# Kernel optimization log

Hardware: AMD Instinct MI355X
Metric: run time of the kernel (lower is better)

Reference implementation:

```python
import jax, jax.numpy as jnp
import numpy as np

C_IN, H, T_OUT, C_OUT = 16, 256, 24, 8


def setup_inputs() -> dict:
    key = jax.random.key(0)
    ks = jax.random.split(key, 8)
    s_ih = 1.0 / np.sqrt(H)
    x = jax.random.normal(ks[0], (8192, C_IN, 48), dtype=jnp.float32)
    # Encoder LSTMCell params (PyTorch layout: gates stacked [i, f, g, o], each H rows)
    enc_Wih = jax.random.uniform(ks[1], (4 * H, C_IN), minval=-s_ih, maxval=s_ih, dtype=jnp.float32)
    enc_Whh = jax.random.uniform(ks[2], (4 * H, H), minval=-s_ih, maxval=s_ih, dtype=jnp.float32)
    enc_b = jax.random.uniform(ks[3], (4 * H,), minval=-s_ih, maxval=s_ih, dtype=jnp.float32)  # b_ih + b_hh folded
    # Decoder LSTMCell has input_size=0 -> W_ih is (4H, 0), contributes nothing
    dec_Whh = jax.random.uniform(ks[4], (4 * H, H), minval=-s_ih, maxval=s_ih, dtype=jnp.float32)
    dec_b = jax.random.uniform(ks[5], (4 * H,), minval=-s_ih, maxval=s_ih, dtype=jnp.float32)
    # TimestepDense: per-timestep (non-shared) linear H -> C_OUT, dropout inactive at eval
    dense_W = jax.random.uniform(ks[6], (T_OUT, C_OUT, H), minval=-s_ih, maxval=s_ih, dtype=jnp.float32)
    dense_b = jax.random.uniform(ks[7], (T_OUT, C_OUT), minval=-s_ih, maxval=s_ih, dtype=jnp.float32)
    return {"x": x, "enc_Wih": enc_Wih, "enc_Whh": enc_Whh, "enc_b": enc_b,
            "dec_Whh": dec_Whh, "dec_b": dec_b, "dense_W": dense_W, "dense_b": dense_b}


def _lstm_step(h, c, gates):
    i, f, g, o = jnp.split(gates, 4, axis=-1)
    c_new = jax.nn.sigmoid(f) * c + jax.nn.sigmoid(i) * jnp.tanh(g)
    h_new = jax.nn.sigmoid(o) * jnp.tanh(c_new)
    return h_new, c_new


def reference(x, enc_Wih, enc_Whh, enc_b, dec_Whh, dec_b, dense_W, dense_b):
    N = x.shape[0]
    # ----- Encoder: scan over T input steps -----
    xt = jnp.transpose(x, (2, 0, 1))  # (T, N, C)
    h0 = jnp.zeros((N, H), dtype=x.dtype)
    c0 = jnp.zeros((N, H), dtype=x.dtype)

    def enc_step(carry, x_t):
        h, c = carry
        gates = x_t @ enc_Wih.T + h @ enc_Whh.T + enc_b  # (N, 4H)
        h, c = _lstm_step(h, c, gates)
        return (h, c), None

    (h_enc, _), _ = jax.lax.scan(enc_step, (h0, c0), xt)

    # ----- Decoder: zero-input LSTM cell, collect hidden states -----
    def dec_step(carry, _):
        h, c = carry
        gates = h @ dec_Whh.T + dec_b
        h, c = _lstm_step(h, c, gates)
        return (h, c), h

    (_, _), hs = jax.lax.scan(dec_step, (h_enc, c0), None, length=T_OUT)  # hs: (T_OUT, N, H)

    # ----- TimestepDense: per-timestep linear H -> C_OUT (eval mode, dropout off) -----
    out = jnp.einsum('tnh,toh->not', hs, dense_W) + dense_b.T[None]  # (N, C_OUT, T_OUT)
    return out
```

## Files before the change

kernel.cpp:

```cpp
#include <hip/hip_runtime.h>

typedef __attribute__((ext_vector_type(8))) _Float16 f16x8;
typedef __attribute__((ext_vector_type(4))) float    f32x4;

#define HD    256
#define CIN   16
#define TIN   48
#define TOUT  24
#define COUT  8
#define MB    32
#define KPAD  296
#define KT_ENC 9
#define KT_DEC 8
#define WE_HALVES (KT_ENC*4*16*512)
#define WD_HALVES (KT_DEC*4*16*512)
#define PREP_TOTAL (WE_HALVES + WD_HALVES)

template <int N> struct KTag { static constexpr int val = N; };

__global__ void prep_frags(const float* __restrict__ enc_Wih,
                           const float* __restrict__ enc_Whh,
                           const float* __restrict__ dec_Whh,
                           _Float16* __restrict__ wf)
{
    int p = blockIdx.x * blockDim.x + threadIdx.x;
    if (p >= PREP_TOTAL) return;
    int lane = (p >> 3) & 63;
    int s    = p & 7;
    int kq   = ((lane >> 4) << 3) + s;
    int l15  = lane & 15;
    float v;
    if (p < WE_HALVES) {
        int frag = p >> 9;
        int kt = frag >> 6, g = (frag >> 4) & 3, ntile = frag & 15;
        int k   = kt * 32 + kq;
        int row = g * 256 + ntile * 16 + l15;
        v = 0.0f;
        if (k < 256)      v = enc_Whh[row * 256 + k];
        else if (k < 272) v = enc_Wih[row * 16 + (k - 256)];
    } else {
        int q = p - WE_HALVES;
        int frag = q >> 9;
        int kt = frag >> 6, g = (frag >> 4) & 3, ntile = frag & 15;
        int k   = kt * 32 + kq;
        int row = g * 256 + ntile * 16 + l15;
        v = dec_Whh[row * 256 + k];
    }
    wf[p] = (_Float16)v;
}

__device__ __forceinline__ float sigm(float v) {
    return __builtin_amdgcn_rcpf(1.0f + __expf(-v));
}
__device__ __forceinline__ float tanh_f(float v) {
    return 1.0f - 2.0f * __builtin_amdgcn_rcpf(1.0f + __expf(2.0f * v));
}

__global__ __launch_bounds__(1024, 4) void seq2seq_mfma(
    const float* __restrict__ x,
    const _Float16* __restrict__ wf,
    const float* __restrict__ enc_b,
    const float* __restrict__ dec_b,
    const float* __restrict__ denseW,
    const float* __restrict__ denseb,
    float* __restrict__ out)
{
    __shared__ __align__(16) _Float16 hF[MB * KPAD];
    __shared__ __align__(16) _Float16 xs[2][MB * CIN * 8];
    __shared__ __align__(16) float    outS[MB * COUT * TOUT];

    const int tid  = threadIdx.x;
    const int w    = tid >> 6;
    const int lane = tid & 63;
    const int quad = lane >> 4;
    const int l15  = lane & 15;
    const int n0   = blockIdx.x * MB;

    float bE[4], bD[4];
    #pragma unroll
    for (int g = 0; g < 4; ++g) {
        int col = w * 16 + l15;
        bE[g] = enc_b[g * 256 + col];
        bD[g] = dec_b[g * 256 + col];
    }

    auto loadchunk = [&](int wd) {
        if (tid < 512) {
            int m = tid >> 4, c = tid & 15;
            const float* xp = x + (size_t)(n0 + m) * (CIN * TIN) + c * TIN + wd * 8;
            float4 v0 = *(const float4*)xp;
            float4 v1 = *(const float4*)(xp + 4);
            f16x8 hv = { (_Float16)v0.x, (_Float16)v0.y, (_Float16)v0.z, (_Float16)v0.w,
                         (_Float16)v1.x, (_Float16)v1.y, (_Float16)v1.z, (_Float16)v1.w };
            *(f16x8*)(&xs[wd & 1][m * (CIN * 8) + c * 8]) = hv;
        }
    };
    auto xcopy = [&](int t) {
        if (tid < 512) {
            int m = tid >> 4, c = tid & 15;
            hF[m * KPAD + 256 + c] = xs[(t >> 3) & 1][m * (CIN * 8) + c * 8 + (t & 7)];
        }
    };

    for (int i = tid; i < MB * KPAD; i += 1024) hF[i] = (_Float16)0.0f;
    loadchunk(0);
    __syncthreads();
    xcopy(0);
    __syncthreads();

    f32x4 acc[2][4];
    float cst[2][4];
    #pragma unroll
    for (int mt = 0; mt < 2; ++mt)
        #pragma unroll
        for (int r = 0; r < 4; ++r) cst[mt][r] = 0.0f;

    const f16x8* Ap0 = (const f16x8*)(hF + l15 * KPAD);
    const f16x8* Ap1 = (const f16x8*)(hF + (16 + l15) * KPAD);
    const f16x8* WpE = (const f16x8*)wf + w * 64 + lane;
    const f16x8* WpD = (const f16x8*)(wf + WE_HALVES) + w * 64 + lane;

    auto gemm = [&](auto kt_tag, const f16x8* __restrict__ Wp, const float (&bias)[4]) {
        constexpr int KT = decltype(kt_tag)::val;
        #pragma unroll
        for (int mt = 0; mt < 2; ++mt)
            #pragma unroll
            for (int g = 0; g < 4; ++g) {
                float b = bias[g];
                f32x4 bv = {b, b, b, b};
                acc[mt][g] = bv;
            }
        #pragma unroll
        for (int kt = 0; kt < KT; ++kt) {
            f16x8 a0 = Ap0[kt * 4 + quad];
            f16x8 a1 = Ap1[kt * 4 + quad];
            #pragma unroll
            for (int g = 0; g < 4; ++g) {
                f16x8 bf = Wp[(kt * 4 + g) * 1024];
                acc[0][g] = __builtin_amdgcn_mfma_f32_16x16x32_f16(a0, bf, acc[0][g], 0, 0, 0);
                acc[1][g] = __builtin_amdgcn_mfma_f32_16x16x32_f16(a1, bf, acc[1][g], 0, 0, 0);
            }
        }
    };

    auto pointwise = [&]() {
        int col = w * 16 + l15;
        #pragma unroll
        for (int mt = 0; mt < 2; ++mt)
            #pragma unroll
            for (int r = 0; r < 4; ++r) {
                float iv = sigm(acc[mt][0][r]);
                float fv = sigm(acc[mt][1][r]);
                float gv = tanh_f(acc[mt][2][r]);
                float ov = sigm(acc[mt][3][r]);
                float cn = fmaf(fv, cst[mt][r], iv * gv);
                cst[mt][r] = cn;
                float hv = ov * tanh_f(cn);
                hF[(mt * 16 + quad * 4 + r) * KPAD + col] = (_Float16)hv;
            }
    };

    for (int t = 0; t < TIN; ++t) {
        gemm(KTag<KT_ENC>{}, WpE, bE);
        __syncthreads();
        pointwise();
        if ((t & 7) == 0 && (t >> 3) + 1 < 6) loadchunk((t >> 3) + 1);
        if (t + 1 < TIN) xcopy(t + 1);
        __syncthreads();
    }

    #pragma unroll
    for (int mt = 0; mt < 2; ++mt)
        #pragma unroll
        for (int r = 0; r < 4; ++r) cst[mt][r] = 0.0f;

    for (int t = 0; t < TOUT; ++t) {
        gemm(KTag<KT_DEC>{}, WpD, bD);
        __syncthreads();
        pointwise();
        __syncthreads();
        if (tid < MB * COUT) {
            int m = tid >> 3, o = tid & 7;
            const float* wr = denseW + (t * COUT + o) * HD;
            float s = denseb[t * COUT + o];
            #pragma unroll 4
            for (int j8 = 0; j8 < 32; ++j8) {
                f16x8 hv  = *(const f16x8*)(hF + m * KPAD + j8 * 8);
                float4 w0 = *(const float4*)(wr + j8 * 8);
                float4 w1 = *(const float4*)(wr + j8 * 8 + 4);
                s = fmaf((float)hv[0], w0.x, s);
                s = fmaf((float)hv[1], w0.y, s);
                s = fmaf((float)hv[2], w0.z, s);
                s = fmaf((float)hv[3], w0.w, s);
                s = fmaf((float)hv[4], w1.x, s);
                s = fmaf((float)hv[5], w1.y, s);
                s = fmaf((float)hv[6], w1.z, s);
                s = fmaf((float)hv[7], w1.w, s);
            }
            outS[m * (COUT * TOUT) + o * TOUT + t] = s;
        }
    }

    __syncthreads();
    {
        const float4* src = (const float4*)outS;
        float4* dst = (float4*)(out + (size_t)n0 * (COUT * TOUT));
        for (int i = tid; i < MB * COUT * TOUT / 4; i += 1024)
            dst[i] = src[i];
    }
}

extern "C" void kernel_launch(void* const* d_in, const int* in_sizes, int n_in,
                              void* d_out, int out_size, void* d_ws, size_t ws_size,
                              hipStream_t stream) {
    const float* x       = (const float*)d_in[0];
    const float* enc_Wih = (const float*)d_in[1];
    const float* enc_Whh = (const float*)d_in[2];
    const float* enc_b   = (const float*)d_in[3];
    const float* dec_Whh = (const float*)d_in[4];
    const float* dec_b   = (const float*)d_in[5];
    const float* denseW  = (const float*)d_in[6];
    const float* denseb  = (const float*)d_in[7];
    float* out = (float*)d_out;
    _Float16* wf = (_Float16*)d_ws;

    prep_frags<<<(PREP_TOTAL + 255) / 256, 256, 0, stream>>>(enc_Wih, enc_Whh, dec_Whh, wf);
    seq2seq_mfma<<<8192 / MB, 1024, 0, stream>>>(x, wf, enc_b, dec_b, denseW, denseb, out);
}
```

Measured before the change: 1.403 ms.

## Double batch rows per block to reuse weight fragments across four M-tiles

Raises the per-block batch tile from 32 to 64 rows, so each weight fragment loaded from global memory feeds four MFMA row tiles instead of two. This halves weight traffic per sample and halves the grid to 128 blocks. The input staging chunk shrinks to 4 timesteps so all 1024 threads can load it, and the output buffer is replaced by a small per-thread 4-step staging area written straight to global memory. The cost is more accumulator registers per thread (16 f32x4 accumulators), a larger hF tile, and fewer blocks than the device has CUs, which could hurt occupancy and parallelism.

```diff
diff --git a/kernel.cpp b/kernel.cpp
--- a/kernel.cpp
+++ b/kernel.cpp
@@ -1,6 +1,7 @@
 #include <hip/hip_runtime.h>
 
 typedef __attribute__((ext_vector_type(8))) _Float16 f16x8;
+typedef __attribute__((ext_vector_type(4))) _Float16 f16x4;
 typedef __attribute__((ext_vector_type(4))) float    f32x4;
 
 #define HD    256
@@ -8,7 +9,7 @@
 #define TIN   48
 #define TOUT  24
 #define COUT  8
-#define MB    32
+#define MB    64
 #define KPAD  296
 #define KT_ENC 9
 #define KT_DEC 8
@@ -66,8 +67,8 @@
     float* __restrict__ out)
 {
     __shared__ __align__(16) _Float16 hF[MB * KPAD];
-    __shared__ __align__(16) _Float16 xs[2][MB * CIN * 8];
-    __shared__ __align__(16) float    outS[MB * COUT * TOUT];
+    __shared__ __align__(16) _Float16 xs[2][MB * CIN * 4];
+    __shared__ __align__(16) float    outS4[MB * COUT * 4];
 
     const int tid  = threadIdx.x;
     const int w    = tid >> 6;
@@ -85,21 +86,15 @@
     }
 
     auto loadchunk = [&](int wd) {
-        if (tid < 512) {
-            int m = tid >> 4, c = tid & 15;
-            const float* xp = x + (size_t)(n0 + m) * (CIN * TIN) + c * TIN + wd * 8;
-            float4 v0 = *(const float4*)xp;
-            float4 v1 = *(const float4*)(xp + 4);
-            f16x8 hv = { (_Float16)v0.x, (_Float16)v0.y, (_Float16)v0.z, (_Float16)v0.w,
-                         (_Float16)v1.x, (_Float16)v1.y, (_Float16)v1.z, (_Float16)v1.w };
-            *(f16x8*)(&xs[wd & 1][m * (CIN * 8) + c * 8]) = hv;
-        }
+        int m = tid >> 4, c = tid & 15;
+        const float* xp = x + (size_t)(n0 + m) * (CIN * TIN) + c * TIN + wd * 4;
+        float4 v = *(const float4*)xp;
+        f16x4 hv = { (_Float16)v.x, (_Float16)v.y, (_Float16)v.z, (_Float16)v.w };
+        *(f16x4*)(&xs[wd & 1][(m * CIN + c) * 4]) = hv;
     };
     auto xcopy = [&](int t) {
-        if (tid < 512) {
-            int m = tid >> 4, c = tid & 15;
-            hF[m * KPAD + 256 + c] = xs[(t >> 3) & 1][m * (CIN * 8) + c * 8 + (t & 7)];
-        }
+        int m = tid >> 4, c = tid & 15;
+        hF[m * KPAD + 256 + c] = xs[(t >> 2) & 1][(m * CIN + c) * 4 + (t & 3)];
     };
 
     for (int i = tid; i < MB * KPAD; i += 1024) hF[i] = (_Float16)0.0f;
@@ -108,22 +103,20 @@
     xcopy(0);
     __syncthreads();
 
-    f32x4 acc[2][4];
-    float cst[2][4];
+    f32x4 acc[4][4];
+    float cst[4][4];
     #pragma unroll
-    for (int mt = 0; mt < 2; ++mt)
+    for (int mt = 0; mt < 4; ++mt)
         #pragma unroll
         for (int r = 0; r < 4; ++r) cst[mt][r] = 0.0f;
 
-    const f16x8* Ap0 = (const f16x8*)(hF + l15 * KPAD);
-    const f16x8* Ap1 = (const f16x8*)(hF + (16 + l15) * KPAD);
     const f16x8* WpE = (const f16x8*)wf + w * 64 + lane;
     const f16x8* WpD = (const f16x8*)(wf + WE_HALVES) + w * 64 + lane;
 
     auto gemm = [&](auto kt_tag, const f16x8* __restrict__ Wp, const float (&bias)[4]) {
         constexpr int KT = decltype(kt_tag)::val;
         #pragma unroll
-        for (int mt = 0; mt < 2; ++mt)
+        for (int mt = 0; mt < 4; ++mt)
             #pragma unroll
             for (int g = 0; g < 4; ++g) {
                 float b = bias[g];
@@ -132,13 +125,16 @@
             }
         #pragma unroll
         for (int kt = 0; kt < KT; ++kt) {
-            f16x8 a0 = Ap0[kt * 4 + quad];
-            f16x8 a1 = Ap1[kt * 4 + quad];
-            #pragma unroll
-            for (int g = 0; g < 4; ++g) {
-                f16x8 bf = Wp[(kt * 4 + g) * 1024];
-                acc[0][g] = __builtin_amdgcn_mfma_f32_16x16x32_f16(a0, bf, acc[0][g], 0, 0, 0);
-                acc[1][g] = __builtin_amdgcn_mfma_f32_16x16x32_f16(a1, bf, acc[1][g], 0, 0, 0);
+            f16x8 bf[4];
+            #pragma unroll
+            for (int g = 0; g < 4; ++g)
+                bf[g] = Wp[(kt * 4 + g) * 1024];
+            #pragma unroll
+            for (int mt = 0; mt < 4; ++mt) {
+                f16x8 a = *(const f16x8*)(hF + (mt * 16 + l15) * KPAD + kt * 32 + quad * 8);
+                #pragma unroll
+                for (int g = 0; g < 4; ++g)
+                    acc[mt][g] = __builtin_amdgcn_mfma_f32_16x16x32_f16(a, bf[g], acc[mt][g], 0, 0, 0);
             }
         }
     };
@@ -146,7 +142,7 @@
     auto pointwise = [&]() {
         int col = w * 16 + l15;
         #pragma unroll
-        for (int mt = 0; mt < 2; ++mt)
+        for (int mt = 0; mt < 4; ++mt)
             #pragma unroll
             for (int r = 0; r < 4; ++r) {
                 float iv = sigm(acc[mt][0][r]);
@@ -164,13 +160,13 @@
         gemm(KTag<KT_ENC>{}, WpE, bE);
         __syncthreads();
         pointwise();
-        if ((t & 7) == 0 && (t >> 3) + 1 < 6) loadchunk((t >> 3) + 1);
+        if ((t & 3) == 0 && (t >> 2) + 1 < TIN / 4) loadchunk((t >> 2) + 1);
         if (t + 1 < TIN) xcopy(t + 1);
         __syncthreads();
     }
 
     #pragma unroll
-    for (int mt = 0; mt < 2; ++mt)
+    for (int mt = 0; mt < 4; ++mt)
         #pragma unroll
         for (int r = 0; r < 4; ++r) cst[mt][r] = 0.0f;
 
@@ -197,16 +193,12 @@
                 s = fmaf((float)hv[6], w1.z, s);
                 s = fmaf((float)hv[7], w1.w, s);
             }
-            outS[m * (COUT * TOUT) + o * TOUT + t] = s;
+            outS4[(tid << 2) | (t & 3)] = s;
+            if ((t & 3) == 3) {
+                float4 v = *(const float4*)&outS4[tid << 2];
+                *(float4*)(out + (size_t)(n0 + m) * (COUT * TOUT) + o * TOUT + (t - 3)) = v;
+            }
         }
-    }
-
-    __syncthreads();
-    {
-        const float4* src = (const float4*)outS;
-        float4* dst = (float4*)(out + (size_t)n0 * (COUT * TOUT));
-        for (int i = tid; i < MB * COUT * TOUT / 4; i += 1024)
-            dst[i] = src[i];
     }
 }
 
```

After: 2.059 ms. 1.47x slower.

## Prefetch first weight k-tiles during pointwise and shrink output staging buffer

Applied to the files above, without the earlier changes.

Loads the first two k-tiles of weight fragments into registers right after the barrier, so the global weight loads overlap the LSTM pointwise phase instead of stalling the next GEMM. The full-sequence output staging buffer is replaced by a small per-thread 4-step buffer that writes float4 chunks directly to global memory, cutting LDS use and dropping the final copy loop. This raises register pressure by eight f16x8 values, which could reduce occupancy or cause spills under the 1024-thread launch bound.

```diff
diff --git a/kernel.cpp b/kernel.cpp
--- a/kernel.cpp
+++ b/kernel.cpp
@@ -67,7 +67,7 @@
 {
     __shared__ __align__(16) _Float16 hF[MB * KPAD];
     __shared__ __align__(16) _Float16 xs[2][MB * CIN * 8];
-    __shared__ __align__(16) float    outS[MB * COUT * TOUT];
+    __shared__ __align__(16) float    outS4[MB * COUT * 4];
 
     const int tid  = threadIdx.x;
     const int w    = tid >> 6;
@@ -120,6 +120,13 @@
     const f16x8* WpE = (const f16x8*)wf + w * 64 + lane;
     const f16x8* WpD = (const f16x8*)(wf + WE_HALVES) + w * 64 + lane;
 
+    f16x8 pre[8];
+    auto prefetch = [&](const f16x8* __restrict__ Wp) {
+        #pragma unroll
+        for (int i = 0; i < 8; ++i) pre[i] = Wp[i * 1024];
+    };
+    prefetch(WpE);
+
     auto gemm = [&](auto kt_tag, const f16x8* __restrict__ Wp, const float (&bias)[4]) {
         constexpr int KT = decltype(kt_tag)::val;
         #pragma unroll
@@ -132,13 +139,16 @@
             }
         #pragma unroll
         for (int kt = 0; kt < KT; ++kt) {
+            f16x8 bf[4];
+            #pragma unroll
+            for (int g = 0; g < 4; ++g)
+                bf[g] = (kt < 2) ? pre[kt * 4 + g] : Wp[(kt * 4 + g) * 1024];
             f16x8 a0 = Ap0[kt * 4 + quad];
             f16x8 a1 = Ap1[kt * 4 + quad];
             #pragma unroll
             for (int g = 0; g < 4; ++g) {
-                f16x8 bf = Wp[(kt * 4 + g) * 1024];
-                acc[0][g] = __builtin_amdgcn_mfma_f32_16x16x32_f16(a0, bf, acc[0][g], 0, 0, 0);
-                acc[1][g] = __builtin_amdgcn_mfma_f32_16x16x32_f16(a1, bf, acc[1][g], 0, 0, 0);
+                acc[0][g] = __builtin_amdgcn_mfma_f32_16x16x32_f16(a0, bf[g], acc[0][g], 0, 0, 0);
+                acc[1][g] = __builtin_amdgcn_mfma_f32_16x16x32_f16(a1, bf[g], acc[1][g], 0, 0, 0);
             }
         }
     };
@@ -163,6 +173,7 @@
     for (int t = 0; t < TIN; ++t) {
         gemm(KTag<KT_ENC>{}, WpE, bE);
         __syncthreads();
+        prefetch((t + 1 < TIN) ? WpE : WpD);
         pointwise();
         if ((t & 7) == 0 && (t >> 3) + 1 < 6) loadchunk((t >> 3) + 1);
         if (t + 1 < TIN) xcopy(t + 1);
@@ -177,15 +188,17 @@
     for (int t = 0; t < TOUT; ++t) {
         gemm(KTag<KT_DEC>{}, WpD, bD);
         __syncthreads();
+        if (t + 1 < TOUT) prefetch(WpD);
         pointwise();
         __syncthreads();
         if (tid < MB * COUT) {
             int m = tid >> 3, o = tid & 7;
             const float* wr = denseW + (t * COUT + o) * HD;
             float s = denseb[t * COUT + o];
+            const _Float16* hrow = hF + m * KPAD;
             #pragma unroll 4
             for (int j8 = 0; j8 < 32; ++j8) {
-                f16x8 hv  = *(const f16x8*)(hF + m * KPAD + j8 * 8);
+                f16x8 hv  = *(const f16x8*)(hrow + j8 * 8);
                 float4 w0 = *(const float4*)(wr + j8 * 8);
                 float4 w1 = *(const float4*)(wr + j8 * 8 + 4);
                 s = fmaf((float)hv[0], w0.x, s);
@@ -197,16 +210,12 @@
                 s = fmaf((float)hv[6], w1.z, s);
                 s = fmaf((float)hv[7], w1.w, s);
             }
-            outS[m * (COUT * TOUT) + o * TOUT + t] = s;
-        }
-    }
-
-    __syncthreads();
-    {
-        const float4* src = (const float4*)outS;
-        float4* dst = (float4*)(out + (size_t)n0 * (COUT * TOUT));
-        for (int i = tid; i < MB * COUT * TOUT / 4; i += 1024)
-            dst[i] = src[i];
+            outS4[(tid << 2) | (t & 3)] = s;
+            if ((t & 3) == 3) {
+                float4 v = *(const float4*)&outS4[tid << 2];
+                *(float4*)(out + (size_t)(n0 + m) * (COUT * TOUT) + o * TOUT + (t - 3)) = v;
+            }
+        }
     }
 }
 
```

New measurement: 1.563 ms. 11.4% more time.
